# Optimization experiments

Hardware: AMD Instinct MI355X
Metric: run time of the kernel (lower is better)

Reference implementation:

```python
import jax, jax.numpy as jnp
import numpy as np

N = 100000      # nodes
IN_DIM = 128    # input feature dim
HID = 64        # hidden_dim / out_dim per head
HEADS = 4
E_RAND = 1600000  # random edges; self-loops appended -> E = E_RAND + N
SCALES = 3


def setup_inputs() -> dict:
    key = jax.random.key(0)
    ks = jax.random.split(key, 12)
    h = jax.random.normal(ks[0], (N, IN_DIM), dtype=jnp.float32)
    src = jax.random.randint(ks[1], (E_RAND,), 0, N)
    dst = jax.random.randint(ks[2], (E_RAND,), 0, N)
    loop = jnp.arange(N)
    src = jnp.concatenate([src, loop])  # self-loops ensure every dst has a mailbox
    dst = jnp.concatenate([dst, loop])
    frac_cover_mat = jax.random.randint(ks[3], (N, SCALES), 0, N)
    # learned params (bias=False everywhere); xavier-ish scaling
    layer1_fc = jax.random.normal(ks[4], (HEADS, HID, IN_DIM), jnp.float32) / np.sqrt(IN_DIM)
    layer1_attn = jax.random.normal(ks[5], (HEADS, 2 * HID), jnp.float32) * 0.1
    layer2_fc = jax.random.normal(ks[6], (HID, HID * HEADS), jnp.float32) / np.sqrt(HID * HEADS)
    layer2_attn = jax.random.normal(ks[7], (2 * HID,), jnp.float32) * 0.1
    frac_w = jax.random.normal(ks[8], (SCALES, HID, IN_DIM), jnp.float32) / np.sqrt(IN_DIM)
    frac_final_w = jax.random.normal(ks[9], (HID, SCALES * HID), jnp.float32) / np.sqrt(SCALES * HID)
    fc2_w = jax.random.normal(ks[10], (HID, 2 * HID), jnp.float32) / np.sqrt(2 * HID)
    return {"h": h, "src": src, "dst": dst, "frac_cover_mat": frac_cover_mat,
            "layer1_fc": layer1_fc, "layer1_attn": layer1_attn,
            "layer2_fc": layer2_fc, "layer2_attn": layer2_attn,
            "frac_w": frac_w, "frac_final_w": frac_final_w, "fc2_w": fc2_w}


def _gat_layer(z, src, dst, attn_w, n):
    # attn(cat([z_src, z_dst])) == z_src @ a_src + z_dst @ a_dst  (bias-free Linear)
    d = z.shape[1]
    e = jax.nn.leaky_relu(z[src] @ attn_w[:d] + z[dst] @ attn_w[d:])  # [E]
    # segment softmax over incoming edges of each dst node
    m = jax.ops.segment_max(e, dst, num_segments=n)
    ex = jnp.exp(e - m[dst])
    denom = jax.ops.segment_sum(ex, dst, num_segments=n)
    alpha = ex / denom[dst]                                   # [E]
    return jax.ops.segment_sum(alpha[:, None] * z[src], dst, num_segments=n)  # [N, d]


def reference(h, src, dst, frac_cover_mat,
              layer1_fc, layer1_attn, layer2_fc, layer2_attn,
              frac_w, frac_final_w, fc2_w):
    n = h.shape[0]
    # layer1: multi-head GAT, merge='cat'
    heads = []
    for i in range(layer1_fc.shape[0]):
        z = h @ layer1_fc[i].T                                # [N, HID]
        heads.append(_gat_layer(z, src, dst, layer1_attn[i], n))
    h_nei = jax.nn.elu(jnp.concatenate(heads, axis=1))        # [N, HID*HEADS]
    # layer2: single-head GAT
    z2 = h_nei @ layer2_fc.T                                  # [N, HID]
    h_nei = _gat_layer(z2, src, dst, layer2_attn, n)          # [N, HID]
    # fractal layer (dropout = identity in eval)
    h_all = [h[frac_cover_mat[:, s]] @ frac_w[s].T for s in range(frac_w.shape[0])]
    h_frac = jnp.concatenate(h_all, axis=1) @ frac_final_w.T  # [N, HID]
    # fc2 on cat([h_nei, h_frac]); dropout identity
    h_global = jnp.concatenate([h_nei, h_frac], axis=1) @ fc2_w.T  # [N, HID]
    # AvgPooling over single graph -> [1, HID]
    return jnp.mean(h_global, axis=0, keepdims=True)
```

## Files before the change

kernel.cpp:

```cpp
#include <hip/hip_runtime.h>
#include <math.h>


#define CAP 128

typedef unsigned int  uint_t;
typedef unsigned short ushort_t;
typedef __attribute__((ext_vector_type(8))) short short8;
typedef __attribute__((ext_vector_type(4))) float floatx4;
typedef __attribute__((ext_vector_type(2))) float floatx2;

__device__ __forceinline__ float wred_sum(float v){
#pragma unroll
  for (int o = 1; o < 64; o <<= 1) v += __shfl_xor(v, o, 64);
  return v;
}
__device__ __forceinline__ float lrelu(float x){ return x >= 0.f ? x : 0.01f*x; }
__device__ __forceinline__ ushort_t f2b(float f){
  uint_t u = __float_as_uint(f);
  u = (u + 0x7FFFu + ((u >> 16) & 1u)) >> 16;
  return (ushort_t)u;
}
__device__ __forceinline__ float b2f_lo(uint_t w){ return __uint_as_float(w << 16); }
__device__ __forceinline__ float b2f_hi(uint_t w){ return __uint_as_float(w & 0xFFFF0000u); }

__global__ void k_prep(const float* __restrict__ W1, const float* __restrict__ W2,
                       const float* __restrict__ a1, const float* __restrict__ a2,
                       const int* __restrict__ dstI, int E,
                       ushort_t* __restrict__ w1bp, float* __restrict__ v2,
                       int* __restrict__ deg){
  __shared__ float v[8][128];
  const int bx = blockIdx.x, t = threadIdx.x;
  if (bx < 128){
    int idx = bx*256 + t;
    int j = idx & 7, lane = (idx >> 3) & 63, ks = (idx >> 9) & 3, tt = idx >> 11;
    int n = tt*16 + (lane & 15), k = ks*32 + (lane >> 4)*8 + j;
    w1bp[idx] = f2b(W1[n*128 + k]);
  } else if (bx == 128){
    for (int o = t; o < 1024; o += 256){
      int col = o >> 7, k = o & 127, hh = col & 3, off = (col >> 2)*64;
      float s = 0.f;
      for (int n = 0; n < 64; n++) s += a1[hh*128 + off + n] * W1[(hh*64 + n)*128 + k];
      v[col][k] = s;
    }
    __syncthreads();
    for (int idx = t; idx < 2048; idx += 256){
      int j = idx & 7, lane = (idx >> 3) & 63, ks = idx >> 9;
      int col = lane & 15, k = ks*32 + (lane >> 4)*8 + j;
      w1bp[32768 + idx] = (col < 8) ? f2b(v[col][k]) : (ushort_t)0;
    }
  } else if (bx == 129){
    float s0 = 0.f, s1 = 0.f;
    for (int j = 0; j < 64; j++){
      float wjk = W2[j*256 + t];
      s0 += wjk * a2[j];
      s1 += wjk * a2[64 + j];
    }
    v2[t] = s0; v2[256 + t] = s1;
  } else {
    const int nb = gridDim.x - 130;
    for (int i = (bx-130)*256 + t; i < E; i += nb*256)
      atomicAdd(&deg[dstI[i]], 1);
  }
}

__global__ __launch_bounds__(256) void k_scan1(const int* __restrict__ deg, int* __restrict__ part){
  __shared__ int tmp[256];
  int t = threadIdx.x;
  tmp[t] = deg[blockIdx.x*256 + t];
  __syncthreads();
  for (int off = 128; off > 0; off >>= 1){
    if (t < off) tmp[t] += tmp[t+off];
    __syncthreads();
  }
  if (t == 0) part[blockIdx.x] = tmp[0];
}
__global__ __launch_bounds__(512) void k_scan2(int* __restrict__ part, int B){
  __shared__ int tmp[512];
  int t = threadIdx.x;
  int v = (t < B) ? part[t] : 0;
  tmp[t] = v; __syncthreads();
  for (int off = 1; off < 512; off <<= 1){
    int x = (t >= off) ? tmp[t-off] : 0;
    __syncthreads();
    tmp[t] += x;
    __syncthreads();
  }
  if (t < B) part[t] = tmp[t] - v;
}
__global__ __launch_bounds__(256) void k_scan3(const int* __restrict__ deg, const int* __restrict__ part,
    int* __restrict__ rowptr, int* __restrict__ cursor){
  __shared__ int tmp[256];
  int t = threadIdx.x, i = blockIdx.x*256 + t;
  int v = deg[i];
  tmp[t] = v; __syncthreads();
  for (int off = 1; off < 256; off <<= 1){
    int x = (t >= off) ? tmp[t-off] : 0;
    __syncthreads();
    tmp[t] += x;
    __syncthreads();
  }
  int excl = tmp[t] - v + part[blockIdx.x];
  rowptr[i] = excl; cursor[i] = excl;
}

__global__ __launch_bounds__(512) void k_mega(const float* __restrict__ h,
    const ushort_t* __restrict__ w1bp,
    uint_t* __restrict__ z8, float* __restrict__ s1s, float* __restrict__ s1d, int N,
    const int* __restrict__ srcI, const int* __restrict__ dstI,
    int* __restrict__ cursor, int* __restrict__ csr, int E, int Gg, int Gs,
    const int* __restrict__ fcm, float* __restrict__ accFrac)
{
  static __shared__ __align__(16) char smem[69632];
  const int bx = blockIdx.x, tid = threadIdx.x;
  if (bx < Gg){
    ushort_t* ldsB = (ushort_t*)smem;
    {
      const uint4* src = (const uint4*)w1bp;
      uint4* dst = (uint4*)ldsB;
      for (int i = tid; i < 4352; i += 512) dst[i] = src[i];
    }
    __syncthreads();
    const int wave = tid >> 6, lane = tid & 63;
    const int quad = lane >> 4, l16 = lane & 15;
    const int row0 = bx*128 + wave*16;
    if (row0 >= N) return;
    const int ar = (row0 + l16 < N) ? (row0 + l16) : (N - 1);
    floatx4 c[17];
#pragma unroll
    for (int t = 0; t < 17; t++) c[t] = (floatx4){0.f,0.f,0.f,0.f};
#pragma unroll
    for (int ks = 0; ks < 4; ks++){
      const float* ap = &h[(size_t)ar*128 + ks*32 + quad*8];
      float4 v0 = *(const float4*)ap;
      float4 v1 = *(const float4*)(ap + 4);
      float vv[8] = {v0.x,v0.y,v0.z,v0.w,v1.x,v1.y,v1.z,v1.w};
      short8 ahi, alo;
#pragma unroll
      for (int j = 0; j < 8; j++){
        ushort_t hb = f2b(vv[j]);
        float hf = __uint_as_float((uint_t)hb << 16);
        ahi[j] = (short)hb;
        alo[j] = (short)f2b(vv[j] - hf);
      }
#pragma unroll
      for (int t = 0; t < 17; t++){
        short8 b = *(const short8*)&ldsB[(size_t)((t*4 + ks)*64 + lane)*8];
        c[t] = __builtin_amdgcn_mfma_f32_16x16x32_bf16(ahi, b, c[t], 0, 0, 0);
      }
      {
        short8 b = *(const short8*)&ldsB[(size_t)((16*4 + ks)*64 + lane)*8];
        c[16] = __builtin_amdgcn_mfma_f32_16x16x32_bf16(alo, b, c[16], 0, 0, 0);
      }
    }
#pragma unroll
    for (int i = 0; i < 4; i++){
      const int r = row0 + quad*4 + i;
      if (r >= N) continue;
#pragma unroll
      for (int m = 0; m < 4; m++){
        int u = 0;
        u = __builtin_amdgcn_cvt_pk_fp8_f32(c[0*4+m][i], c[1*4+m][i], u, false);
        u = __builtin_amdgcn_cvt_pk_fp8_f32(c[2*4+m][i], c[3*4+m][i], u, true);
        z8[(size_t)r*64 + m*16 + l16] = (uint_t)u;
      }
      const float sv = c[16][i];
      if (l16 < 4) s1s[r*4 + l16] = sv;
      else if (l16 < 8) s1d[r*4 + (l16 - 4)] = sv;
    }
  } else if (bx < Gg + Gs){
    const int i = (bx - Gg)*512 + tid;
    if (i < E){
      int p = atomicAdd(&cursor[dstI[i]], 1);
      csr[p] = srcI[i];
    }
  } else {
    float (*red)[384] = (float(*)[384])smem;
    const int wave = tid >> 6, lane = tid & 63;
    const int g = lane >> 5, li = lane & 31;
    const int Gf = gridDim.x - Gg - Gs;
    const int stream0 = (bx - Gg - Gs)*16 + wave*2 + g;
    const int step = Gf * 16;
    float4 a0 = {0,0,0,0}, a1 = {0,0,0,0}, a2 = {0,0,0,0};
    for (int n = stream0; n < N; n += step){
      int i0 = fcm[n*3], i1 = fcm[n*3+1], i2 = fcm[n*3+2];
      float4 v0 = *(const float4*)&h[(size_t)i0*128 + li*4];
      float4 v1 = *(const float4*)&h[(size_t)i1*128 + li*4];
      float4 v2 = *(const float4*)&h[(size_t)i2*128 + li*4];
      a0.x += v0.x; a0.y += v0.y; a0.z += v0.z; a0.w += v0.w;
      a1.x += v1.x; a1.y += v1.y; a1.z += v1.z; a1.w += v1.w;
      a2.x += v2.x; a2.y += v2.y; a2.z += v2.z; a2.w += v2.w;
    }
    const int w16 = wave*2 + g;
    *(float4*)&red[w16][0*128 + li*4] = a0;
    *(float4*)&red[w16][1*128 + li*4] = a1;
    *(float4*)&red[w16][2*128 + li*4] = a2;
    __syncthreads();
    for (int i = tid; i < 384; i += 512){
      float v = 0.f;
#pragma unroll
      for (int w = 0; w < 16; w++) v += red[w][i];
      atomicAdd(&accFrac[i], v);
    }
  }
}

__global__ __launch_bounds__(256) void k_gat1(
    const uint_t* __restrict__ z8, const float* __restrict__ s1src, const float* __restrict__ s1dst,
    const int* __restrict__ rowptr, const int* __restrict__ csr, const float* __restrict__ v2,
    uint_t* __restrict__ hneib, float* __restrict__ s2s, float* __restrict__ s2d, int N)
{
  __shared__ int   sbuf[4][CAP];
  __shared__ __align__(16) float4 ebuf[4][CAP];
  __shared__ float v2s[512];
  const int tid = threadIdx.x;
  v2s[tid] = v2[tid];
  v2s[tid + 256] = v2[tid + 256];
  __syncthreads();
  const int wave = tid >> 6, lane = tid & 63;
  const int dst = blockIdx.x*4 + wave;
  if (dst >= N) return;
  const int beg = rowptr[dst];
  const int deg = rowptr[dst+1] - beg;
  const float4 sd = *(const float4*)&s1dst[dst*4];
  float t0=0.f,t1=0.f,t2=0.f,t3=0.f;
  for (int j = lane; j < deg; j += 64){
    int s = csr[beg+j];
    float4 sv = *(const float4*)&s1src[s*4];
    float4 a;
    a.x = __expf(lrelu(sv.x+sd.x)); a.y = __expf(lrelu(sv.y+sd.y));
    a.z = __expf(lrelu(sv.z+sd.z)); a.w = __expf(lrelu(sv.w+sd.w));
    if (j < CAP){ sbuf[wave][j] = s; ebuf[wave][j] = a; }
    t0 += a.x; t1 += a.y; t2 += a.z; t3 += a.w;
  }
  const float inv[4] = {1.f/wred_sum(t0), 1.f/wred_sum(t1), 1.f/wred_sum(t2), 1.f/wred_sum(t3)};
  const int eh = lane >> 5, li = lane & 31;
  float acc[2][4] = {};
  int jj = 0;
  if (deg <= CAP){
    for (; jj + 2 <= deg; jj += 2){
      const int j = jj + eh;
      int s = sbuf[wave][j]; float4 al = ebuf[wave][j];
      uint2 u = *((const uint2*)(z8 + (size_t)s*64) + li);
      floatx2 p0 = __builtin_amdgcn_cvt_pk_f32_fp8(u.x, false);
      floatx2 p1 = __builtin_amdgcn_cvt_pk_f32_fp8(u.x, true);
      floatx2 p2 = __builtin_amdgcn_cvt_pk_f32_fp8(u.y, false);
      floatx2 p3 = __builtin_amdgcn_cvt_pk_f32_fp8(u.y, true);
      acc[0][0] += al.x * p0.x;
      acc[0][1] += al.y * p0.y;
      acc[0][2] += al.z * p1.x;
      acc[0][3] += al.w * p1.y;
      acc[1][0] += al.x * p2.x;
      acc[1][1] += al.y * p2.y;
      acc[1][2] += al.z * p3.x;
      acc[1][3] += al.w * p3.y;
    }
    if (jj < deg && eh == 0){
      int s = sbuf[wave][jj]; float4 al = ebuf[wave][jj];
      uint2 u = *((const uint2*)(z8 + (size_t)s*64) + li);
      floatx2 p0 = __builtin_amdgcn_cvt_pk_f32_fp8(u.x, false);
      floatx2 p1 = __builtin_amdgcn_cvt_pk_f32_fp8(u.x, true);
      floatx2 p2 = __builtin_amdgcn_cvt_pk_f32_fp8(u.y, false);
      floatx2 p3 = __builtin_amdgcn_cvt_pk_f32_fp8(u.y, true);
      acc[0][0] += al.x * p0.x;
      acc[0][1] += al.y * p0.y;
      acc[0][2] += al.z * p1.x;
      acc[0][3] += al.w * p1.y;
      acc[1][0] += al.x * p2.x;
      acc[1][1] += al.y * p2.y;
      acc[1][2] += al.z * p3.x;
      acc[1][3] += al.w * p3.y;
    }
  } else {
    for (; jj < deg; jj += 2){
      const int j = jj + eh;
      const bool v = j < deg;
      const int jc = v ? j : jj;
      int s; float4 al;
      if (jc < CAP){ s = sbuf[wave][jc]; al = ebuf[wave][jc]; }
      else {
        s = csr[beg+jc];
        float4 sv = *(const float4*)&s1src[s*4];
        al.x = __expf(lrelu(sv.x+sd.x)); al.y = __expf(lrelu(sv.y+sd.y));
        al.z = __expf(lrelu(sv.z+sd.z)); al.w = __expf(lrelu(sv.w+sd.w));
      }
      if (!v){ al.x=0.f; al.y=0.f; al.z=0.f; al.w=0.f; }
      uint2 u = *((const uint2*)(z8 + (size_t)s*64) + li);
      floatx2 p0 = __builtin_amdgcn_cvt_pk_f32_fp8(u.x, false);
      floatx2 p1 = __builtin_amdgcn_cvt_pk_f32_fp8(u.x, true);
      floatx2 p2 = __builtin_amdgcn_cvt_pk_f32_fp8(u.y, false);
      floatx2 p3 = __builtin_amdgcn_cvt_pk_f32_fp8(u.y, true);
      acc[0][0] += al.x * p0.x;
      acc[0][1] += al.y * p0.y;
      acc[0][2] += al.z * p1.x;
      acc[0][3] += al.w * p1.y;
      acc[1][0] += al.x * p2.x;
      acc[1][1] += al.y * p2.y;
      acc[1][2] += al.z * p3.x;
      acc[1][3] += al.w * p3.y;
    }
  }
#pragma unroll
  for (int k = 0; k < 2; k++)
#pragma unroll
    for (int hh = 0; hh < 4; hh++) acc[k][hh] += __shfl_xor(acc[k][hh], 32, 64);
  const float* vv = &v2s[eh*256];
  float p = 0.f;
#pragma unroll
  for (int hh = 0; hh < 4; hh++){
    float e0 = acc[0][hh]*inv[hh]; e0 = e0 > 0.f ? e0 : expm1f(e0);
    float e1 = acc[1][hh]*inv[hh]; e1 = e1 > 0.f ? e1 : expm1f(e1);
    p += e0 * vv[hh*64 + 2*li] + e1 * vv[hh*64 + 2*li + 1];
    if (eh == 0)
      hneib[(size_t)dst*128 + hh*32 + li] = (uint_t)f2b(e0) | ((uint_t)f2b(e1) << 16);
  }
#pragma unroll
  for (int o = 1; o < 32; o <<= 1) p += __shfl_xor(p, o, 64);
  if (lane == 0)  s2s[dst] = p;
  if (lane == 32) s2d[dst] = p;
}

__global__ __launch_bounds__(256) void k_aw2(
    const float* __restrict__ s2s, const float* __restrict__ s2d,
    const int* __restrict__ rowptr, const int* __restrict__ csr,
    float* __restrict__ wsrc, int N)
{
  __shared__ int   sbuf[4][CAP];
  __shared__ float ebuf[4][CAP];
  const int wave = threadIdx.x >> 6, lane = threadIdx.x & 63;
  const int dst = blockIdx.x*4 + wave;
  if (dst >= N) return;
  const int beg = rowptr[dst], deg = rowptr[dst+1] - beg;
  const float sd = s2d[dst];
  float ts = 0.f;
  for (int j = lane; j < deg; j += 64){
    int s = csr[beg+j];
    float a = __expf(lrelu(s2s[s] + sd));
    if (j < CAP){ sbuf[wave][j] = s; ebuf[wave][j] = a; }
    ts += a;
  }
  const float inv = 1.f/wred_sum(ts);
  for (int j = lane; j < deg; j += 64){
    int s; float a;
    if (j < CAP){ s = sbuf[wave][j]; a = ebuf[wave][j]; }
    else { s = csr[beg+j]; a = __expf(lrelu(s2s[s] + sd)); }
    atomicAdd(&wsrc[s], a * inv);
  }
}

__global__ __launch_bounds__(256) void k_hsum(const uint_t* __restrict__ hneib,
    const float* __restrict__ wsrc, float* __restrict__ acc256, int N)
{
  __shared__ float pr[512];
  const int t = threadIdx.x;
  const int h2 = t >> 7, p = t & 127;
  float a0 = 0.f, a1 = 0.f;
  const int step = gridDim.x * 2;
  for (int n = blockIdx.x*2 + h2; n < N; n += step){
    float wn = wsrc[n];
    uint_t u = hneib[(size_t)n*128 + p];
    a0 += wn * b2f_lo(u);
    a1 += wn * b2f_hi(u);
  }
  pr[h2*256 + 2*p]     = a0;
  pr[h2*256 + 2*p + 1] = a1;
  __syncthreads();
  float v = pr[t] + pr[256 + t];
  int pp = t >> 1;
  int d = (pp >> 5)*64 + 2*(pp & 31) + (t & 1);
  atomicAdd(&acc256[d], v);
}

__global__ __launch_bounds__(256) void k_finalize(const float* __restrict__ acc256,
    const float* __restrict__ accFrac, const float* __restrict__ W2,
    const float* __restrict__ frw, const float* __restrict__ frf,
    const float* __restrict__ fc2, float* __restrict__ out, float invN)
{
  __shared__ float mh[256], nei[64], g[384], mm[192], hfrac[64];
  int t = threadIdx.x;
  mh[t] = acc256[t] * invN;
  for (int i = t; i < 384; i += 256) g[i] = accFrac[i] * invN;
  __syncthreads();
  if (t < 64){
    float s = 0.f;
    for (int k = 0; k < 256; k++) s += W2[t*256 + k] * mh[k];
    nei[t] = s;
  }
  for (int i = t; i < 192; i += 256){
    int s = i >> 6, d = i & 63;
    const float* w = frw + (size_t)(s*64 + d)*128;
    const float* gs = g + s*128;
    float sum = 0.f;
    for (int k = 0; k < 128; k++) sum += gs[k]*w[k];
    mm[i] = sum;
  }
  __syncthreads();
  if (t < 64){
    float s = 0.f;
    for (int k = 0; k < 192; k++) s += mm[k]*frf[t*192 + k];
    hfrac[t] = s;
  }
  __syncthreads();
  if (t < 64){
    float o = 0.f;
    for (int k = 0; k < 64; k++)
      o += fc2[t*128 + k]*nei[k] + fc2[t*128 + 64 + k]*hfrac[k];
    out[t] = o;
  }
}

extern "C" void kernel_launch(void* const* d_in, const int* in_sizes, int n_in,
                              void* d_out, int out_size, void* d_ws, size_t ws_size,
                              hipStream_t stream)
{
  const float* h    = (const float*)d_in[0];
  const int*   srcI = (const int*)  d_in[1];
  const int*   dstI = (const int*)  d_in[2];
  const int*   fcm  = (const int*)  d_in[3];
  const float* l1fc = (const float*)d_in[4];
  const float* l1at = (const float*)d_in[5];
  const float* l2fc = (const float*)d_in[6];
  const float* l2at = (const float*)d_in[7];
  const float* frw  = (const float*)d_in[8];
  const float* frf  = (const float*)d_in[9];
  const float* fc2  = (const float*)d_in[10];
  float* out = (float*)d_out;
  (void)n_in; (void)out_size; (void)ws_size;

  const int N = in_sizes[0] / 128;
  const int E = in_sizes[1];
  const int B = (N + 256) / 256;
  const int PAD = B * 256;

  char* w = (char*)d_ws;
  size_t off = 0;
  auto alloc = [&](size_t bytes) -> char* {
    char* p = w + off; off = (off + bytes + 255) & ~(size_t)255; return p;
  };
  uint_t* z8    = (uint_t*)alloc((size_t)N*64*4);
  uint_t* hneib = (uint_t*)alloc((size_t)N*128*4);
  float* s1s  = (float*)alloc((size_t)N*4*4);
  float* s1d  = (float*)alloc((size_t)N*4*4);
  float* s2s  = (float*)alloc((size_t)N*4);
  float* s2d  = (float*)alloc((size_t)N*4);
  int*   deg     = (int*)  alloc((size_t)PAD*4);
  float* wsrc    = (float*)alloc((size_t)N*4);
  float* acc256  = (float*)alloc(256*4);
  float* accFrac = (float*)alloc(384*4);
  const size_t zbytes = (size_t)((char*)accFrac + 384*4 - (char*)deg);
  int*   rowptr = (int*)alloc((size_t)PAD*4);
  int*   cursor = (int*)alloc((size_t)PAD*4);
  int*   part   = (int*)alloc(512*4);
  int*   csr    = (int*)alloc((size_t)E*4);
  ushort_t* w1bp = (ushort_t*)alloc(34816*2);
  float* v2     = (float*)alloc(512*4);

  hipMemsetAsync(deg, 0, zbytes, stream);

  hipLaunchKernelGGL(k_prep,  dim3(130 + 512), dim3(256), 0, stream,
                     l1fc, l2fc, l1at, l2at, dstI, E, w1bp, v2, deg);
  hipLaunchKernelGGL(k_scan1, dim3(B),   dim3(256), 0, stream, deg, part);
  hipLaunchKernelGGL(k_scan2, dim3(1),   dim3(512), 0, stream, part, B);
  hipLaunchKernelGGL(k_scan3, dim3(B),   dim3(256), 0, stream, deg, part, rowptr, cursor);

  const int Gg = (N + 127) / 128;
  const int Gs = (E + 511) / 512;
  const int Gf = 512;
  hipLaunchKernelGGL(k_mega,  dim3(Gg + Gs + Gf), dim3(512), 0, stream,
                     h, w1bp, z8, s1s, s1d, N,
                     srcI, dstI, cursor, csr, E, Gg, Gs,
                     fcm, accFrac);
  hipLaunchKernelGGL(k_gat1,  dim3((N+3)/4), dim3(256), 0, stream,
                     z8, s1s, s1d, rowptr, csr, v2, hneib, s2s, s2d, N);
  hipLaunchKernelGGL(k_aw2,   dim3((N+3)/4), dim3(256), 0, stream,
                     s2s, s2d, rowptr, csr, wsrc, N);
  hipLaunchKernelGGL(k_hsum,  dim3(608),     dim3(256), 0, stream,
                     hneib, wsrc, acc256, N);
  hipLaunchKernelGGL(k_finalize, dim3(1),    dim3(256), 0, stream,
                     acc256, accFrac, l2fc, frw, frf, fc2, out, 1.0f/(float)N);
}
```

Baseline: 614.7 us.

## Interleave mega-kernel block roles and halve GEMM LDS footprint for occupancy

The fused kernel's block indices are remapped with a coprime golden-ratio stride, so GEMM, CSR-scatter and fractal-gather blocks are interleaved across the launch instead of running in contiguous phases. The weight tiles are permuted in prep so the GEMM can load half of the B matrix into LDS at a time. This cuts static shared memory from about 68KB to 36KB and the accumulator count from 17 to 9, with the aim of raising occupancy and overlapping memory-bound and compute-bound work. The cost is an extra LDS reload and barrier per block, and the h rows are re-read and re-split for the second half.

Result: faster. 532.4 us (-13.4%).

```diff
diff --git a/kernel.cpp b/kernel.cpp
--- a/kernel.cpp
+++ b/kernel.cpp
@@ -35,7 +35,9 @@
     int idx = bx*256 + t;
     int j = idx & 7, lane = (idx >> 3) & 63, ks = (idx >> 9) & 3, tt = idx >> 11;
     int n = tt*16 + (lane & 15), k = ks*32 + (lane >> 4)*8 + j;
-    w1bp[idx] = f2b(W1[n*128 + k]);
+    int hh = tt >> 2, m = tt & 3;
+    int pt = (m < 2) ? (hh*2 + m) : (8 + hh*2 + (m - 2));
+    w1bp[((pt*4 + ks)*64 + lane)*8 + j] = f2b(W1[n*128 + k]);
   } else if (bx == 128){
     for (int o = t; o < 1024; o += 256){
       int col = o >> 7, k = o & 127, hh = col & 3, off = (col >> 2)*64;
@@ -108,68 +110,79 @@
     const ushort_t* __restrict__ w1bp,
     uint_t* __restrict__ z8, float* __restrict__ s1s, float* __restrict__ s1d, int N,
     const int* __restrict__ srcI, const int* __restrict__ dstI,
-    int* __restrict__ cursor, int* __restrict__ csr, int E, int Gg, int Gs,
+    int* __restrict__ cursor, int* __restrict__ csr, int E,
+    int Gg, int Gs, int G, int step,
     const int* __restrict__ fcm, float* __restrict__ accFrac)
 {
-  static __shared__ __align__(16) char smem[69632];
-  const int bx = blockIdx.x, tid = threadIdx.x;
-  if (bx < Gg){
+  static __shared__ __align__(16) char smem[36864];
+  const int tid = threadIdx.x;
+  const int id = (int)(((unsigned long long)blockIdx.x * (unsigned)step) % (unsigned)G);
+  if (id < Gg){
     ushort_t* ldsB = (ushort_t*)smem;
-    {
-      const uint4* src = (const uint4*)w1bp;
-      uint4* dst = (uint4*)ldsB;
-      for (int i = tid; i < 4352; i += 512) dst[i] = src[i];
-    }
-    __syncthreads();
     const int wave = tid >> 6, lane = tid & 63;
     const int quad = lane >> 4, l16 = lane & 15;
-    const int row0 = bx*128 + wave*16;
-    if (row0 >= N) return;
-    const int ar = (row0 + l16 < N) ? (row0 + l16) : (N - 1);
-    floatx4 c[17];
-#pragma unroll
-    for (int t = 0; t < 17; t++) c[t] = (floatx4){0.f,0.f,0.f,0.f};
-#pragma unroll
-    for (int ks = 0; ks < 4; ks++){
-      const float* ap = &h[(size_t)ar*128 + ks*32 + quad*8];
-      float4 v0 = *(const float4*)ap;
-      float4 v1 = *(const float4*)(ap + 4);
-      float vv[8] = {v0.x,v0.y,v0.z,v0.w,v1.x,v1.y,v1.z,v1.w};
-      short8 ahi, alo;
-#pragma unroll
-      for (int j = 0; j < 8; j++){
-        ushort_t hb = f2b(vv[j]);
-        float hf = __uint_as_float((uint_t)hb << 16);
-        ahi[j] = (short)hb;
-        alo[j] = (short)f2b(vv[j] - hf);
+    const int row0 = id*128 + wave*16;
+    const bool act = row0 < N;
+    const int ar = act ? ((row0 + l16 < N) ? (row0 + l16) : (N - 1)) : 0;
+#pragma unroll
+    for (int half = 0; half < 2; half++){
+      __syncthreads();
+      {
+        const int cnt = half ? 2304 : 2048;
+        const uint4* src = (const uint4*)w1bp + (half ? 2048 : 0);
+        uint4* dst = (uint4*)ldsB;
+        for (int i = tid; i < cnt; i += 512) dst[i] = src[i];
       }
-#pragma unroll
-      for (int t = 0; t < 17; t++){
-        short8 b = *(const short8*)&ldsB[(size_t)((t*4 + ks)*64 + lane)*8];
-        c[t] = __builtin_amdgcn_mfma_f32_16x16x32_bf16(ahi, b, c[t], 0, 0, 0);
+      __syncthreads();
+      if (!act) continue;
+      const int nt = half ? 9 : 8;
+      floatx4 c[9];
+#pragma unroll
+      for (int i = 0; i < 9; i++) c[i] = (floatx4){0.f,0.f,0.f,0.f};
+#pragma unroll
+      for (int ks = 0; ks < 4; ks++){
+        const float* ap = &h[(size_t)ar*128 + ks*32 + quad*8];
+        float4 v0 = *(const float4*)ap;
+        float4 v1 = *(const float4*)(ap + 4);
+        float vv[8] = {v0.x,v0.y,v0.z,v0.w,v1.x,v1.y,v1.z,v1.w};
+        short8 ahi, alo;
+#pragma unroll
+        for (int j = 0; j < 8; j++){
+          ushort_t hb = f2b(vv[j]);
+          float hf = __uint_as_float((uint_t)hb << 16);
+          ahi[j] = (short)hb;
+          alo[j] = (short)f2b(vv[j] - hf);
+        }
+        for (int i = 0; i < nt; i++){
+          short8 b = *(const short8*)&ldsB[(size_t)((i*4 + ks)*64 + lane)*8];
+          c[i] = __builtin_amdgcn_mfma_f32_16x16x32_bf16(ahi, b, c[i], 0, 0, 0);
+        }
+        if (half){
+          short8 b = *(const short8*)&ldsB[(size_t)((8*4 + ks)*64 + lane)*8];
+          c[8] = __builtin_amdgcn_mfma_f32_16x16x32_bf16(alo, b, c[8], 0, 0, 0);
+        }
       }
-      {
-        short8 b = *(const short8*)&ldsB[(size_t)((16*4 + ks)*64 + lane)*8];
-        c[16] = __builtin_amdgcn_mfma_f32_16x16x32_bf16(alo, b, c[16], 0, 0, 0);
+      const int m0 = half ? 2 : 0;
+#pragma unroll
+      for (int i = 0; i < 4; i++){
+        const int r = row0 + quad*4 + i;
+        if (r >= N) continue;
+#pragma unroll
+        for (int dm = 0; dm < 2; dm++){
+          int u = 0;
+          u = __builtin_amdgcn_cvt_pk_fp8_f32(c[0*2+dm][i], c[1*2+dm][i], u, false);
+          u = __builtin_amdgcn_cvt_pk_fp8_f32(c[2*2+dm][i], c[3*2+dm][i], u, true);
+          z8[(size_t)r*64 + (m0+dm)*16 + l16] = (uint_t)u;
+        }
+        if (half){
+          const float sv = c[8][i];
+          if (l16 < 4) s1s[r*4 + l16] = sv;
+          else if (l16 < 8) s1d[r*4 + (l16 - 4)] = sv;
+        }
       }
     }
-#pragma unroll
-    for (int i = 0; i < 4; i++){
-      const int r = row0 + quad*4 + i;
-      if (r >= N) continue;
-#pragma unroll
-      for (int m = 0; m < 4; m++){
-        int u = 0;
-        u = __builtin_amdgcn_cvt_pk_fp8_f32(c[0*4+m][i], c[1*4+m][i], u, false);
-        u = __builtin_amdgcn_cvt_pk_fp8_f32(c[2*4+m][i], c[3*4+m][i], u, true);
-        z8[(size_t)r*64 + m*16 + l16] = (uint_t)u;
-      }
-      const float sv = c[16][i];
-      if (l16 < 4) s1s[r*4 + l16] = sv;
-      else if (l16 < 8) s1d[r*4 + (l16 - 4)] = sv;
-    }
-  } else if (bx < Gg + Gs){
-    const int i = (bx - Gg)*512 + tid;
+  } else if (id < Gg + Gs){
+    const int i = (id - Gg)*512 + tid;
     if (i < E){
       int p = atomicAdd(&cursor[dstI[i]], 1);
       csr[p] = srcI[i];
@@ -178,11 +191,11 @@
     float (*red)[384] = (float(*)[384])smem;
     const int wave = tid >> 6, lane = tid & 63;
     const int g = lane >> 5, li = lane & 31;
-    const int Gf = gridDim.x - Gg - Gs;
-    const int stream0 = (bx - Gg - Gs)*16 + wave*2 + g;
-    const int step = Gf * 16;
+    const int Gf = G - Gg - Gs;
+    const int stream0 = (id - Gg - Gs)*16 + wave*2 + g;
+    const int step16 = Gf * 16;
     float4 a0 = {0,0,0,0}, a1 = {0,0,0,0}, a2 = {0,0,0,0};
-    for (int n = stream0; n < N; n += step){
+    for (int n = stream0; n < N; n += step16){
       int i0 = fcm[n*3], i1 = fcm[n*3+1], i2 = fcm[n*3+2];
       float4 v0 = *(const float4*)&h[(size_t)i0*128 + li*4];
       float4 v1 = *(const float4*)&h[(size_t)i1*128 + li*4];
@@ -466,9 +479,14 @@
   const int Gg = (N + 127) / 128;
   const int Gs = (E + 511) / 512;
   const int Gf = 512;
-  hipLaunchKernelGGL(k_mega,  dim3(Gg + Gs + Gf), dim3(512), 0, stream,
+  const int G  = Gg + Gs + Gf;
+  int step = (int)(G * 0.618) | 1;
+  auto gcd = [](int a, int b){ while (b){ int t = a % b; a = b; b = t; } return a; };
+  while (gcd(step, G) != 1) step += 2;
+
+  hipLaunchKernelGGL(k_mega,  dim3(G), dim3(512), 0, stream,
                      h, w1bp, z8, s1s, s1d, N,
-                     srcI, dstI, cursor, csr, E, Gg, Gs,
+                     srcI, dstI, cursor, csr, E, Gg, Gs, G, step,
                      fcm, accFrac);
   hipLaunchKernelGGL(k_gat1,  dim3((N+3)/4), dim3(256), 0, stream,
                      z8, s1s, s1d, rowptr, csr, v2, hneib, s2s, s2d, N);
```
